# Kernel optimization log

Measured on AMD Instinct MI355X. Metric: run time of the kernel, lower is better.

## Reference

```python
import jax, jax.numpy as jnp
import numpy as np

N = 200000      # nodes
E_EDGES = 600000
G = 8000        # graphs
F_IN = 16
EMB = 128
L = 5           # GIN layers
C = 12          # targets
BN_EPS = 1e-5


def _bn(x, s, b, m, v):
    # BatchNorm1d in eval mode: normalize with stored running stats
    return (x - m) * jax.lax.rsqrt(v + BN_EPS) * s + b


def _mlp(x, w1, b1, s1, bb1, m1, v1, w2, b2, s2, bb2, m2, v2):
    h = jax.nn.relu(_bn(x @ w1 + b1, s1, bb1, m1, v1))
    return jax.nn.relu(_bn(h @ w2 + b2, s2, bb2, m2, v2))


def setup_inputs() -> dict:
    key = jax.random.key(0)
    ks = iter(jax.random.split(key, 64))
    inp = {}
    def nrm(shape, fan):
        return (jax.random.normal(next(ks), shape, jnp.float32) / np.sqrt(fan)).astype(jnp.float32)
    def bn_set(name, shape):
        inp[name + '_scale'] = jax.random.uniform(next(ks), shape, jnp.float32) * 0.5 + 0.75
        inp[name + '_bias'] = jax.random.normal(next(ks), shape, jnp.float32) * 0.1
        inp[name + '_mean'] = jax.random.normal(next(ks), shape, jnp.float32) * 0.1
        inp[name + '_var'] = jax.random.uniform(next(ks), shape, jnp.float32) * 0.5 + 0.75

    inp['x'] = jax.random.normal(next(ks), (N, F_IN), jnp.float32)
    src = jax.random.randint(next(ks), (E_EDGES,), 0, N, jnp.int32)
    dst = jax.random.randint(next(ks), (E_EDGES,), 0, N, jnp.int32)
    inp['edge_index'] = jnp.stack([src, dst])
    # sorted batch ids; every graph gets at least one node (avoid empty segment_max)
    inp['batch'] = jnp.sort(jnp.concatenate([
        jnp.arange(G, dtype=jnp.int32),
        jax.random.randint(next(ks), (N - G,), 0, G, jnp.int32)]))

    inp['init_w1'] = nrm((F_IN, EMB), F_IN)
    inp['init_b1'] = jnp.zeros((EMB,), jnp.float32)
    bn_set('init_bn1', (EMB,))
    inp['init_w2'] = nrm((EMB, EMB), EMB)
    inp['init_b2'] = jnp.zeros((EMB,), jnp.float32)
    bn_set('init_bn2', (EMB,))
    inp['init_lin_w'] = nrm((EMB, C), EMB)
    inp['init_lin_b'] = jnp.zeros((C,), jnp.float32)
    inp['eps'] = jnp.zeros((L,), jnp.float32)  # train_eps init 0.0
    inp['lw1'] = nrm((L, EMB, EMB), EMB)
    inp['lb1'] = jnp.zeros((L, EMB), jnp.float32)
    bn_set('lbn1', (L, EMB))
    inp['lw2'] = nrm((L, EMB, EMB), EMB)
    inp['lb2'] = jnp.zeros((L, EMB), jnp.float32)
    bn_set('lbn2', (L, EMB))
    inp['llin_w'] = nrm((L, EMB, C), EMB)
    inp['llin_b'] = jnp.zeros((L, C), jnp.float32)
    return inp


def _forward(edge_index, batch, x, init_w1, init_b1, init_bn1_scale, init_bn1_bias,
             init_bn1_mean, init_bn1_var, init_w2, init_b2, init_bn2_scale,
             init_bn2_bias, init_bn2_mean, init_bn2_var, init_lin_w, init_lin_b,
             eps, lw1, lb1, lbn1_scale, lbn1_bias, lbn1_mean, lbn1_var,
             lw2, lb2, lbn2_scale, lbn2_bias, lbn2_mean, lbn2_var, llin_w, llin_b):
    src, dst = edge_index[0], edge_index[1]
    h = _mlp(x, init_w1, init_b1, init_bn1_scale, init_bn1_bias, init_bn1_mean,
             init_bn1_var, init_w2, init_b2, init_bn2_scale, init_bn2_bias,
             init_bn2_mean, init_bn2_var)  # [N, EMB]
    # initial readout: linear then global max pool over graphs
    out = jax.ops.segment_max(h @ init_lin_w + init_lin_b, batch, num_segments=G)  # [G, C]
    for l in range(L):
        # GINConv: h <- MLP((1+eps)*h + sum_{j in N(i)} h_j)
        agg = jax.ops.segment_sum(h[src], dst, num_segments=N)  # gather + scatter-add
        h = _mlp((1.0 + eps[l]) * h + agg,
                 lw1[l], lb1[l], lbn1_scale[l], lbn1_bias[l], lbn1_mean[l], lbn1_var[l],
                 lw2[l], lb2[l], lbn2_scale[l], lbn2_bias[l], lbn2_mean[l], lbn2_var[l])
        # per-layer readout: global max pool then linear
        out = out + jax.ops.segment_max(h, batch, num_segments=G) @ llin_w[l] + llin_b[l]
    return out


def reference(x, edge_index, batch, init_w1, init_b1, init_bn1_scale, init_bn1_bias,
              init_bn1_mean, init_bn1_var, init_w2, init_b2, init_bn2_scale,
              init_bn2_bias, init_bn2_mean, init_bn2_var, init_lin_w, init_lin_b,
              eps, lw1, lb1, lbn1_scale, lbn1_bias, lbn1_mean, lbn1_var,
              lw2, lb2, lbn2_scale, lbn2_bias, lbn2_mean, lbn2_var, llin_w, llin_b):
    return _forward(edge_index, batch, x, init_w1, init_b1, init_bn1_scale,
                    init_bn1_bias, init_bn1_mean, init_bn1_var, init_w2, init_b2,
                    init_bn2_scale, init_bn2_bias, init_bn2_mean, init_bn2_var,
                    init_lin_w, init_lin_b, eps, lw1, lb1, lbn1_scale, lbn1_bias,
                    lbn1_mean, lbn1_var, lw2, lb2, lbn2_scale, lbn2_bias,
                    lbn2_mean, lbn2_var, llin_w, llin_b)
```

## Files before the change

### kernel.cpp

```cpp
#include <hip/hip_runtime.h>
#include <hip/hip_bf16.h>
#include <math.h>

#define EMB 128
#define CDIM 12
#define FIN 16
#define NLAYER 5
#define BN_EPS 1e-5f

typedef __attribute__((ext_vector_type(8))) _Float16 f16x8;
typedef __attribute__((ext_vector_type(2))) __fp16 fp16v2;
typedef __attribute__((ext_vector_type(4))) float f32x4;
typedef unsigned short ushort_t;

union h2u { fp16v2 h; unsigned u; };
union hu  { _Float16 h; ushort_t u; };

__device__ __forceinline__ unsigned pkrn(float x, float y) {
    hu A; A.h = (_Float16)x;
    hu B; B.h = (_Float16)y;
    return (unsigned)A.u | ((unsigned)B.u << 16);
}

__device__ __forceinline__ unsigned swz(int node, unsigned byteoff) {
    return (unsigned)(node * 256 + byteoff) ^ (((unsigned)node & 7u) << 4);
}


__global__ __launch_bounds__(256) void k_gstart(const int* __restrict__ batch,
                                                int* __restrict__ gs, int N, int G) {
    int i = blockIdx.x * 256 + threadIdx.x;
    if (i >= N) return;
    if (i == 0) gs[0] = 0;
    else { int b = batch[i]; if (b != batch[i - 1]) gs[b] = i; }
    if (i == N - 1) gs[G] = N;
}

__global__ __launch_bounds__(256) void k_zero_i32(int* __restrict__ p, int n) {
    int i = blockIdx.x * 256 + threadIdx.x;
    if (i < n) p[i] = 0;
}

__global__ __launch_bounds__(256) void k_fill_i32(int* __restrict__ p, int val, int n) {
    int i = blockIdx.x * 256 + threadIdx.x;
    if (i < n) p[i] = val;
}

__global__ __launch_bounds__(256) void k_zero_f32(float* __restrict__ p, int n) {
    int i = blockIdx.x * 256 + threadIdx.x;
    if (i < n) p[i] = 0.f;
}

__global__ __launch_bounds__(128) void k_zero_dummy(ushort_t* __restrict__ a,
                                                    ushort_t* __restrict__ b, int N) {
    int i = threadIdx.x;
    a[(size_t)N * EMB + i] = 0;
    b[(size_t)N * EMB + i] = 0;
}

__global__ __launch_bounds__(256) void k_hist(const int* __restrict__ dst, int* __restrict__ cnt, int E) {
    int e = blockIdx.x * 256 + threadIdx.x;
    if (e < E) atomicAdd(&cnt[dst[e]], 1);
}

__global__ __launch_bounds__(256) void k_scan1(const int* __restrict__ cnt, int* __restrict__ rs,
                                               int* __restrict__ partials, int N) {
    __shared__ int tsum[256];
    int t = threadIdx.x;
    int base = blockIdx.x * 1024 + t * 4;
    int c[4];
    #pragma unroll
    for (int j = 0; j < 4; j++) c[j] = (base + j < N) ? ((cnt[base + j] + 3) & ~3) : 0;
    int s = c[0] + c[1] + c[2] + c[3];
    tsum[t] = s;
    __syncthreads();
    for (int off = 1; off < 256; off <<= 1) {
        int v = (t >= off) ? tsum[t - off] : 0;
        __syncthreads();
        tsum[t] += v;
        __syncthreads();
    }
    int run = tsum[t] - s;
    if (t == 255) partials[blockIdx.x] = tsum[255];
    #pragma unroll
    for (int j = 0; j < 4; j++) {
        if (base + j <= N) rs[base + j] = run;
        run += c[j];
    }
}

__global__ __launch_bounds__(256) void k_scan2(int* __restrict__ partials, int NB) {
    __shared__ int tmp[256];
    int t = threadIdx.x;
    int v = (t < NB) ? partials[t] : 0;
    tmp[t] = v;
    __syncthreads();
    for (int off = 1; off < 256; off <<= 1) {
        int u = (t >= off) ? tmp[t - off] : 0;
        __syncthreads();
        tmp[t] += u;
        __syncthreads();
    }
    if (t < NB) partials[t] = tmp[t] - v;
}

__global__ __launch_bounds__(256) void k_scan3(int* __restrict__ rs, const int* __restrict__ partials,
                                               int* __restrict__ cur_off, int N) {
    int t = threadIdx.x;
    int base = blockIdx.x * 1024 + t * 4;
    int add = partials[blockIdx.x];
    #pragma unroll
    for (int j = 0; j < 4; j++) {
        int i = base + j;
        if (i <= N) {
            int v = rs[i] + add;
            rs[i] = v;
            if (i < N) cur_off[i] = v;
        }
    }
}

__global__ __launch_bounds__(256) void k_fillslots(const int* __restrict__ src, const int* __restrict__ dst,
                                                   int* __restrict__ cur_off, int* __restrict__ csr_src, int E) {
    int e = blockIdx.x * 256 + threadIdx.x;
    if (e >= E) return;
    int d = dst[e];
    int pos = atomicAdd(&cur_off[d], 1);
    csr_src[pos] = src[e];
}


__global__ __launch_bounds__(256) void k_prep(
        const float* __restrict__ init_w1, const float* __restrict__ init_b1,
        const float* __restrict__ b1s, const float* __restrict__ b1b,
        const float* __restrict__ b1m, const float* __restrict__ b1v,
        const float* __restrict__ init_w2, const float* __restrict__ init_b2,
        const float* __restrict__ i_s, const float* __restrict__ i_b,
        const float* __restrict__ i_m, const float* __restrict__ i_v,
        const float* __restrict__ lw1, const float* __restrict__ lb1,
        const float* __restrict__ l1s, const float* __restrict__ l1b,
        const float* __restrict__ l1m, const float* __restrict__ l1v,
        const float* __restrict__ lw2, const float* __restrict__ lb2,
        const float* __restrict__ l2s, const float* __restrict__ l2b,
        const float* __restrict__ l2m, const float* __restrict__ l2v,
        const float* __restrict__ ilin_w, const float* __restrict__ ilin_b,
        ushort_t* __restrict__ WT, float* __restrict__ biasf,
        float* __restrict__ W1f, float* __restrict__ bias1f,
        ushort_t* __restrict__ WzT, float* __restrict__ biasz) {
    int j = blockIdx.x;
    int t = threadIdx.x;
    __shared__ float alpha[EMB];

    if (j == 12) {
        if (t < 16) biasz[t] = (t < CDIM) ? ilin_b[t] : 0.f;
        for (int i = t; i < 16 * EMB; i += 256) {
            int f = i >> 7, k = i & 127;
            float w = (f < CDIM) ? ilin_w[k * CDIM + f] : 0.f;
            hu x; x.h = (_Float16)w;
            WzT[i] = x.u;
        }
        return;
    }
    if (j == 11) {
        if (t < EMB) {
            float a = b1s[t] * rsqrtf(b1v[t] + BN_EPS);
            alpha[t] = a;
            bias1f[t] = init_b1[t] * a + (b1b[t] - b1m[t] * a);
        }
        __syncthreads();
        for (int i = t; i < FIN * EMB; i += 256) W1f[i] = init_w1[i] * alpha[i & 127];
        return;
    }

    const float *W, *lb, *s, *bb, *m, *v;
    if (j == 0)      { W = init_w2;            lb = init_b2;        s = i_s;           bb = i_b;           m = i_m;           v = i_v; }
    else if (j <= 5) { int l = j - 1; W = lw1 + l * 16384; lb = lb1 + l * 128; s = l1s + l * 128; bb = l1b + l * 128; m = l1m + l * 128; v = l1v + l * 128; }
    else             { int l = j - 6; W = lw2 + l * 16384; lb = lb2 + l * 128; s = l2s + l * 128; bb = l2b + l * 128; m = l2m + l * 128; v = l2v + l * 128; }
    if (t < EMB) {
        float a = s[t] * rsqrtf(v[t] + BN_EPS);
        alpha[t] = a;
        biasf[j * EMB + t] = lb[t] * a + (bb[t] - m[t] * a);
    }
    __syncthreads();
    for (int i = t; i < EMB * EMB; i += 256) {
        int k = i >> 7, f = i & 127;
        float w = W[i] * alpha[f];
        hu x; x.h = (_Float16)w;
        WT[j * 16384 + f * 128 + k] = x.u;
    }
}


template<int MODE>
__global__ __launch_bounds__(512, 4) void k_layer(
        const float* __restrict__ xin, const ushort_t* __restrict__ hin,
        ushort_t* __restrict__ hout, float* __restrict__ z,
        const ushort_t* __restrict__ W1T, const float* __restrict__ b1,
        const ushort_t* __restrict__ W2T, const float* __restrict__ b2,
        const ushort_t* __restrict__ WzT, const float* __restrict__ bz,
        const float* __restrict__ W1f, const float* __restrict__ b1f,
        const int* __restrict__ rs, const int* __restrict__ csr, const float* __restrict__ epsp,
        const int* __restrict__ batch, float* __restrict__ smax,
        int ntiles, int N) {
    constexpr int NT = (MODE == 1) ? 32 : 16;
    __shared__ ushort_t Aq[NT * 128], Bq[NT * 128];
    __shared__ float W1s[(MODE == 0) ? FIN * EMB : 1];

    const int t = threadIdx.x;
    const int w = t >> 6;
    const int lane = t & 63;
    const int col = lane & 15, kg = lane >> 4;

    if (MODE == 0) {
        for (int i = t; i < FIN * EMB; i += 512) W1s[i] = W1f[i];
        __syncthreads();
    }

    f16x8 w1f[4], w2f[4], wzf[4];
    #pragma unroll
    for (int s = 0; s < 4; s++) {
        int off = (w * 16 + col) * EMB + s * 32 + kg * 8;
        w1f[s] = *(const f16x8*)(W1T + off);
        if (MODE == 1) w2f[s] = *(const f16x8*)(W2T + off);
        if (MODE == 0) {
            int zoff = col * EMB + s * 32 + kg * 8;
            wzf[s] = *(const f16x8*)(WzT + zoff);
        }
    }
    float4 bv1 = *(const float4*)&b1[w * 16 + kg * 4];
    float4 bv2, bvz;
    if (MODE == 1) bv2 = *(const float4*)&b2[w * 16 + kg * 4];
    if (MODE == 0) bvz = *(const float4*)&bz[kg * 4];
    float se = (MODE == 1) ? (1.f + epsp[0]) : 0.f;
    _Float16 seh = (_Float16)se;

    for (int tile = blockIdx.x; tile < ntiles; tile += gridDim.x) {
        const int n0 = tile * NT;

        if (MODE == 1) {
            const int nl = t >> 4, q2 = t & 15;
            const int nc = min(n0 + nl, N - 1);
            const f16x8* hp = (const f16x8*)hin;
            f16x8 acc = hp[(size_t)nc * 16 + q2];
            f16x8 sev = {seh, seh, seh, seh, seh, seh, seh, seh};
            acc = acc * sev;
            int p = rs[nc], pe = rs[nc + 1];
            for (; p < pe; p += 4) {
                uint4 idx = *(const uint4*)&csr[p];
                f16x8 v0 = hp[(size_t)idx.x * 16 + q2];
                f16x8 v1 = hp[(size_t)idx.y * 16 + q2];
                f16x8 v2 = hp[(size_t)idx.z * 16 + q2];
                f16x8 v3 = hp[(size_t)idx.w * 16 + q2];
                acc = acc + v0 + v1 + v2 + v3;
            }
            *(f16x8*)((char*)Aq + swz(nl, (unsigned)q2 * 16)) = acc;
        } else {
            const int nl = t >> 5, q = t & 31;
            const int nc = min(n0 + nl, N - 1);
            float4 ba = *(const float4*)&b1f[q * 4];
            float a0 = ba.x, a1 = ba.y, a2 = ba.z, a3 = ba.w;
            const float* xp = xin + (size_t)nc * FIN;
            #pragma unroll
            for (int k = 0; k < FIN; k++) {
                float xk = xp[k];
                float4 wv = *(const float4*)&W1s[k * EMB + q * 4];
                a0 += xk * wv.x; a1 += xk * wv.y; a2 += xk * wv.z; a3 += xk * wv.w;
            }
            a0 = fmaxf(a0, 0.f); a1 = fmaxf(a1, 0.f); a2 = fmaxf(a2, 0.f); a3 = fmaxf(a3, 0.f);
            uint2 H;
            H.x = pkrn(a0, a1); H.y = pkrn(a2, a3);
            *(uint2*)((char*)Aq + swz(nl, (unsigned)q * 8)) = H;
        }
        __syncthreads();

        {
            f32x4 aA0 = (f32x4){0.f, 0.f, 0.f, 0.f}, aA1 = aA0;
            #pragma unroll
            for (int s = 0; s < 4; s++) {
                unsigned bo = (unsigned)((s * 32 + kg * 8) * 2);
                f16x8 x0 = *(const f16x8*)((const char*)Aq + swz(col, bo));
                aA0 = __builtin_amdgcn_mfma_f32_16x16x32_f16(w1f[s], x0, aA0, 0, 0, 0);
                if (MODE == 1) {
                    f16x8 x1 = *(const f16x8*)((const char*)Aq + swz(col + 16, bo));
                    aA1 = __builtin_amdgcn_mfma_f32_16x16x32_f16(w1f[s], x1, aA1, 0, 0, 0);
                }
            }
            #pragma unroll
            for (int sub = 0; sub < ((MODE == 1) ? 2 : 1); sub++) {
                f32x4 aa = sub ? aA1 : aA0;
                float y0 = fmaxf(aa[0] + bv1.x, 0.f);
                float y1 = fmaxf(aa[1] + bv1.y, 0.f);
                float y2 = fmaxf(aa[2] + bv1.z, 0.f);
                float y3 = fmaxf(aa[3] + bv1.w, 0.f);
                uint2 P; P.x = pkrn(y0, y1); P.y = pkrn(y2, y3);
                if (MODE == 0) {
                    int onode = n0 + col;
                    if (onode < N)
                        *(uint2*)&hout[(size_t)onode * EMB + w * 16 + kg * 4] = P;
                }
                *(uint2*)((char*)Bq + swz(col + sub * 16, (unsigned)(w * 32 + kg * 8))) = P;
            }
        }
        __syncthreads();

        if (MODE == 1) {
            f32x4 aA0 = (f32x4){0.f, 0.f, 0.f, 0.f}, aA1 = aA0;
            #pragma unroll
            for (int s = 0; s < 4; s++) {
                unsigned bo = (unsigned)((s * 32 + kg * 8) * 2);
                f16x8 x0 = *(const f16x8*)((const char*)Bq + swz(col, bo));
                f16x8 x1 = *(const f16x8*)((const char*)Bq + swz(col + 16, bo));
                aA0 = __builtin_amdgcn_mfma_f32_16x16x32_f16(w2f[s], x0, aA0, 0, 0, 0);
                aA1 = __builtin_amdgcn_mfma_f32_16x16x32_f16(w2f[s], x1, aA1, 0, 0, 0);
            }
            #pragma unroll
            for (int sub = 0; sub < 2; sub++) {
                f32x4 aa = sub ? aA1 : aA0;
                int onode = n0 + col + sub * 16;
                float o0 = fmaxf(aa[0] + bv2.x, 0.f);
                float o1 = fmaxf(aa[1] + bv2.y, 0.f);
                float o2 = fmaxf(aa[2] + bv2.z, 0.f);
                float o3 = fmaxf(aa[3] + bv2.w, 0.f);
                if (hout && onode < N) {
                    uint2 P; P.x = pkrn(o0, o1); P.y = pkrn(o2, o3);
                    *(uint2*)&hout[(size_t)onode * EMB + w * 16 + kg * 4] = P;
                }
                bool valid = onode < N;
                float v0 = valid ? o0 : 0.f, v1 = valid ? o1 : 0.f;
                float v2 = valid ? o2 : 0.f, v3 = valid ? o3 : 0.f;
                int g = batch[min(onode, N - 1)];
                #pragma unroll
                for (int off = 1; off < 16; off <<= 1) {
                    float u0 = __shfl_up(v0, off, 16);
                    float u1 = __shfl_up(v1, off, 16);
                    float u2 = __shfl_up(v2, off, 16);
                    float u3 = __shfl_up(v3, off, 16);
                    int gg = __shfl_up(g, off, 16);
                    bool take = (col >= off) && (gg == g);
                    if (take) {
                        v0 = fmaxf(v0, u0); v1 = fmaxf(v1, u1);
                        v2 = fmaxf(v2, u2); v3 = fmaxf(v3, u3);
                    }
                }
                int gn = __shfl_down(g, 1, 16);
                bool tail = (col == 15) || (gn != g);
                if (tail) {
                    unsigned* sp = (unsigned*)&smax[(size_t)g * EMB + w * 16 + kg * 4];
                    atomicMax(sp + 0, __float_as_uint(v0));
                    atomicMax(sp + 1, __float_as_uint(v1));
                    atomicMax(sp + 2, __float_as_uint(v2));
                    atomicMax(sp + 3, __float_as_uint(v3));
                }
            }
        } else if (w == 0) {
            f32x4 aA0 = (f32x4){0.f, 0.f, 0.f, 0.f};
            #pragma unroll
            for (int s = 0; s < 4; s++) {
                unsigned bo = (unsigned)((s * 32 + kg * 8) * 2);
                f16x8 x0 = *(const f16x8*)((const char*)Bq + swz(col, bo));
                aA0 = __builtin_amdgcn_mfma_f32_16x16x32_f16(wzf[s], x0, aA0, 0, 0, 0);
            }
            int onode = n0 + col;
            if (onode < N && kg < 3) {
                float4 o;
                o.x = aA0[0] + bvz.x;
                o.y = aA0[1] + bvz.y;
                o.z = aA0[2] + bvz.z;
                o.w = aA0[3] + bvz.w;
                *(float4*)&z[(size_t)onode * CDIM + kg * 4] = o;
            }
        }
    }
}


__global__ __launch_bounds__(64) void k_zmax(const float* __restrict__ z, const int* __restrict__ gs,
        float* __restrict__ out, int G) {
    int g = blockIdx.x;
    int t = threadIdx.x;
    if (t >= CDIM) return;
    int s0 = gs[g], e0 = gs[g + 1];
    float m = -INFINITY;
    for (int n = s0; n < e0; n++) m = fmaxf(m, z[(size_t)n * CDIM + t]);
    out[g * CDIM + t] = m;
}

__global__ __launch_bounds__(128) void k_comb(const float* __restrict__ smax,
        const float* __restrict__ llin_w, const float* __restrict__ llin_b,
        float* __restrict__ out, int G) {
    int g = blockIdx.x;
    int t = threadIdx.x;
    __shared__ float mv[NLAYER][EMB];
    #pragma unroll
    for (int l = 0; l < NLAYER; l++)
        mv[l][t] = smax[((size_t)l * G + g) * EMB + t];
    __syncthreads();
    __shared__ float parts_[8][16];
    int c = t & 15, half = t >> 4;
    float acc = 0.f;
    if (c < CDIM) {
        #pragma unroll
        for (int l = 0; l < NLAYER; l++) {
            const float* Wl = llin_w + l * EMB * CDIM;
            #pragma unroll
            for (int kk = 0; kk < 16; kk++) {
                int k = half * 16 + kk;
                acc += mv[l][k] * Wl[k * CDIM + c];
            }
        }
    }
    parts_[half][c] = acc;
    __syncthreads();
    if (t < CDIM) {
        float s = 0.f;
        #pragma unroll
        for (int hh = 0; hh < 8; hh++) s += parts_[hh][t];
        #pragma unroll
        for (int l = 0; l < NLAYER; l++) s += llin_b[l * CDIM + t];
        out[g * CDIM + t] += s;
    }
}


extern "C" void kernel_launch(void* const* d_in, const int* in_sizes, int n_in,
                              void* d_out, int out_size, void* d_ws, size_t ws_size,
                              hipStream_t stream) {
    const float* x        = (const float*)d_in[0];
    const int*   ei       = (const int*)d_in[1];
    const int*   batch    = (const int*)d_in[2];
    const float* init_w1  = (const float*)d_in[3];
    const float* init_b1  = (const float*)d_in[4];
    const float* ibn1_s   = (const float*)d_in[5];
    const float* ibn1_b   = (const float*)d_in[6];
    const float* ibn1_m   = (const float*)d_in[7];
    const float* ibn1_v   = (const float*)d_in[8];
    const float* init_w2  = (const float*)d_in[9];
    const float* init_b2  = (const float*)d_in[10];
    const float* ibn2_s   = (const float*)d_in[11];
    const float* ibn2_b   = (const float*)d_in[12];
    const float* ibn2_m   = (const float*)d_in[13];
    const float* ibn2_v   = (const float*)d_in[14];
    const float* ilin_w   = (const float*)d_in[15];
    const float* ilin_b   = (const float*)d_in[16];
    const float* eps      = (const float*)d_in[17];
    const float* lw1      = (const float*)d_in[18];
    const float* lb1      = (const float*)d_in[19];
    const float* lbn1_s   = (const float*)d_in[20];
    const float* lbn1_b   = (const float*)d_in[21];
    const float* lbn1_m   = (const float*)d_in[22];
    const float* lbn1_v   = (const float*)d_in[23];
    const float* lw2      = (const float*)d_in[24];
    const float* lb2      = (const float*)d_in[25];
    const float* lbn2_s   = (const float*)d_in[26];
    const float* lbn2_b   = (const float*)d_in[27];
    const float* lbn2_m   = (const float*)d_in[28];
    const float* lbn2_v   = (const float*)d_in[29];
    const float* llin_w   = (const float*)d_in[30];
    const float* llin_b   = (const float*)d_in[31];

    const int N = in_sizes[0] / FIN;
    const int E = in_sizes[1] / 2;
    const int G = out_size / CDIM;
    const int* src = ei;
    const int* dst = ei + E;
    float* out = (float*)d_out;

    const int EPADMAX = E + 3 * N;

    char* wp = (char*)d_ws;
    auto alloc = [&](size_t bytes) { char* p = wp; wp += (bytes + 255) & ~(size_t)255; return p; };
    ushort_t* WT    = (ushort_t*)alloc((size_t)11 * 16384 * 2);
    float*    biasf = (float*)alloc(11 * EMB * 4);
    float*    W1f   = (float*)alloc(FIN * EMB * 4);
    float*    bias1f= (float*)alloc(EMB * 4);
    ushort_t* WzT   = (ushort_t*)alloc(16 * EMB * 2);
    float*    biasz = (float*)alloc(16 * 4);
    int*      gs    = (int*)alloc((size_t)(G + 1) * 4);
    int*      rs    = (int*)alloc((size_t)(N + 1) * 4);
    int*      curoff= (int*)alloc((size_t)N * 4);
    int*      csr   = (int*)alloc((size_t)EPADMAX * 4);
    int*      parts = (int*)alloc(256 * 4);
    float*    zbuf  = (float*)alloc((size_t)N * CDIM * 4);
    float*    smax  = (float*)alloc((size_t)NLAYER * G * EMB * 4);
    ushort_t* bufP  = (ushort_t*)alloc((size_t)(N + 1) * EMB * 2);
    ushort_t* bufQ  = (ushort_t*)alloc((size_t)(N + 1) * EMB * 2);
    int*      cnt   = csr;

    const int NB = (N + 1 + 1023) / 1024;
    const int ntiles16 = (N + 15) / 16;
    const int ntiles32 = (N + 31) / 32;
    const int GRID = 2084;

    k_zero_f32<<<((NLAYER * G * EMB) + 255) / 256, 256, 0, stream>>>(smax, NLAYER * G * EMB);
    k_zero_dummy<<<1, 128, 0, stream>>>(bufP, bufQ, N);

    k_zero_i32<<<(N + 255) / 256, 256, 0, stream>>>(cnt, N);
    k_hist<<<(E + 255) / 256, 256, 0, stream>>>(dst, cnt, E);
    k_scan1<<<NB, 256, 0, stream>>>(cnt, rs, parts, N);
    k_scan2<<<1, 256, 0, stream>>>(parts, NB);
    k_scan3<<<NB, 256, 0, stream>>>(rs, parts, curoff, N);
    k_fill_i32<<<(EPADMAX + 255) / 256, 256, 0, stream>>>(csr, N, EPADMAX);
    k_fillslots<<<(E + 255) / 256, 256, 0, stream>>>(src, dst, curoff, csr, E);
    k_gstart<<<(N + 255) / 256, 256, 0, stream>>>(batch, gs, N, G);
    k_prep<<<13, 256, 0, stream>>>(init_w1, init_b1, ibn1_s, ibn1_b, ibn1_m, ibn1_v,
                                   init_w2, init_b2, ibn2_s, ibn2_b, ibn2_m, ibn2_v,
                                   lw1, lb1, lbn1_s, lbn1_b, lbn1_m, lbn1_v,
                                   lw2, lb2, lbn2_s, lbn2_b, lbn2_m, lbn2_v,
                                   ilin_w, ilin_b,
                                   WT, biasf, W1f, bias1f, WzT, biasz);

    k_layer<0><<<GRID, 512, 0, stream>>>(x, nullptr, bufQ, zbuf,
                                         WT, biasf,
                                         nullptr, nullptr,
                                         WzT, biasz,
                                         W1f, bias1f,
                                         nullptr, nullptr, nullptr,
                                         nullptr, nullptr, ntiles16, N);
    k_zmax<<<G, 64, 0, stream>>>(zbuf, gs, out, G);

    ushort_t* cur = bufQ;
    ushort_t* oth = bufP;
    for (int l = 0; l < NLAYER; l++) {
        ushort_t* houtl = (l == NLAYER - 1) ? nullptr : oth;
        k_layer<1><<<GRID, 512, 0, stream>>>(nullptr, cur, houtl, nullptr,
                                             WT + (size_t)(1 + l) * 16384, biasf + (1 + l) * EMB,
                                             WT + (size_t)(6 + l) * 16384, biasf + (6 + l) * EMB,
                                             nullptr, nullptr,
                                             nullptr, nullptr,
                                             rs, csr, eps + l,
                                             batch, smax + (size_t)l * G * EMB, ntiles32, N);
        ushort_t* tmp = cur; cur = oth; oth = tmp;
    }
    k_comb<<<G, 128, 0, stream>>>(smax, llin_w, llin_b, out, G);
}
```

Baseline: 659.0 us.

## Use contiguous tile ranges and carry per-graph max across tiles to cut atomics

In the layer kernel, each block now handles a contiguous range of tiles instead of striding across the grid. The running segment max of the last graph in each 16-node group is carried in registers into the next group, and is written with atomicMax only when the graph id changes or the block finishes. This removes many redundant atomics to the pooled-max buffer for graphs that span group boundaries. In exchange it adds shuffles and control flow per group, and contiguous assignment may change load balance and memory access locality.

```diff
diff --git a/kernel.cpp b/kernel.cpp
--- a/kernel.cpp
+++ b/kernel.cpp
@@ -234,7 +234,20 @@
     float se = (MODE == 1) ? (1.f + epsp[0]) : 0.f;
     _Float16 seh = (_Float16)se;
 
-    for (int tile = blockIdx.x; tile < ntiles; tile += gridDim.x) {
+    int t0, t1, tstep;
+    if (MODE == 1) {
+        int tpb = (ntiles + (int)gridDim.x - 1) / (int)gridDim.x;
+        t0 = blockIdx.x * tpb;
+        t1 = min(t0 + tpb, ntiles);
+        tstep = 1;
+    } else {
+        t0 = blockIdx.x; t1 = ntiles; tstep = gridDim.x;
+    }
+
+    int car_g = -1;
+    float car0 = 0.f, car1 = 0.f, car2 = 0.f, car3 = 0.f;
+
+    for (int tile = t0; tile < t1; tile += tstep) {
         const int n0 = tile * NT;
 
         if (MODE == 1) {
@@ -329,6 +342,18 @@
                 float v0 = valid ? o0 : 0.f, v1 = valid ? o1 : 0.f;
                 float v2 = valid ? o2 : 0.f, v3 = valid ? o3 : 0.f;
                 int g = batch[min(onode, N - 1)];
+                int g_first = __shfl(g, 0, 16);
+                if (car_g >= 0 && g_first != car_g) {
+                    if (col == 0) {
+                        unsigned* sp = (unsigned*)&smax[(size_t)car_g * EMB + w * 16 + kg * 4];
+                        atomicMax(sp + 0, __float_as_uint(car0));
+                        atomicMax(sp + 1, __float_as_uint(car1));
+                        atomicMax(sp + 2, __float_as_uint(car2));
+                        atomicMax(sp + 3, __float_as_uint(car3));
+                    }
+                    car_g = -1;
+                }
+                bool inherit = (car_g == g_first);
                 #pragma unroll
                 for (int off = 1; off < 16; off <<= 1) {
                     float u0 = __shfl_up(v0, off, 16);
@@ -342,15 +367,23 @@
                         v2 = fmaxf(v2, u2); v3 = fmaxf(v3, u3);
                     }
                 }
+                float m0 = v0, m1 = v1, m2 = v2, m3 = v3;
+                if (inherit && g == g_first) {
+                    m0 = fmaxf(m0, car0); m1 = fmaxf(m1, car1);
+                    m2 = fmaxf(m2, car2); m3 = fmaxf(m3, car3);
+                }
                 int gn = __shfl_down(g, 1, 16);
-                bool tail = (col == 15) || (gn != g);
-                if (tail) {
+                bool tail = (gn != g);
+                if (tail && col != 15) {
                     unsigned* sp = (unsigned*)&smax[(size_t)g * EMB + w * 16 + kg * 4];
-                    atomicMax(sp + 0, __float_as_uint(v0));
-                    atomicMax(sp + 1, __float_as_uint(v1));
-                    atomicMax(sp + 2, __float_as_uint(v2));
-                    atomicMax(sp + 3, __float_as_uint(v3));
-                }
+                    atomicMax(sp + 0, __float_as_uint(m0));
+                    atomicMax(sp + 1, __float_as_uint(m1));
+                    atomicMax(sp + 2, __float_as_uint(m2));
+                    atomicMax(sp + 3, __float_as_uint(m3));
+                }
+                car0 = __shfl(m0, 15, 16); car1 = __shfl(m1, 15, 16);
+                car2 = __shfl(m2, 15, 16); car3 = __shfl(m3, 15, 16);
+                car_g = __shfl(g, 15, 16);
             }
         } else if (w == 0) {
             f32x4 aA0 = (f32x4){0.f, 0.f, 0.f, 0.f};
@@ -370,6 +403,14 @@
                 *(float4*)&z[(size_t)onode * CDIM + kg * 4] = o;
             }
         }
+    }
+
+    if (MODE == 1 && car_g >= 0 && col == 0) {
+        unsigned* sp = (unsigned*)&smax[(size_t)car_g * EMB + w * 16 + kg * 4];
+        atomicMax(sp + 0, __float_as_uint(car0));
+        atomicMax(sp + 1, __float_as_uint(car1));
+        atomicMax(sp + 2, __float_as_uint(car2));
+        atomicMax(sp + 3, __float_as_uint(car3));
     }
 }
 
```

Result: no change. 670.8 us (+1.8%).
